# Performance work log

Measured on AMD Instinct MI355X. Metric: run time of the kernel, lower is better.

The kernel has to match this reference:

```python
import jax, jax.numpy as jnp
import numpy as np

EPS = 1e-7  # tf.keras.backend.epsilon()
ROUTINGS = 3


def setup_inputs() -> dict:
    key = jax.random.key(0)
    k1, k2 = jax.random.split(key)
    x = jax.random.normal(k1, (64, 2048, 8), dtype=jnp.float32)
    W = jax.random.normal(k2, (32, 2048, 16, 8), dtype=jnp.float32) * 0.05
    return {"x": x, "W": W}


def _squash(s):
    # source squash: vectors / sqrt(sum(v^2) + eps)
    ssq = jnp.sum(s * s, axis=-1, keepdims=True)
    return s / jnp.sqrt(ssq + EPS)


def reference(x, W):
    # x: [B, N, I]; W: [J, N, D, I]
    # prediction vectors u_hat: [B, J, N, D]
    u_hat = jnp.einsum('bni,jndi->bjnd', x, W)
    b = jnp.zeros(u_hat.shape[:-1], dtype=u_hat.dtype)  # [B, J, N]
    v = None
    for i in range(ROUTINGS):
        c = jax.nn.softmax(b, axis=1)                       # coupling over output caps J
        s = jnp.einsum('bjnd,bjn->bjd', u_hat, c)           # weighted sum over input caps N
        v = _squash(s)                                      # [B, J, D]
        if i < ROUTINGS - 1:
            b = b + jnp.einsum('bjnd,bjd->bjn', u_hat, v)   # agreement update
    return v
```

## Files before the change

kernel.cpp:

```cpp
#include <hip/hip_runtime.h>


#define BB_ 64
#define NN_ 2048
#define II_ 8
#define JJ_ 32
#define DD_ 16
#define NCHUNKS 128
#define CHUNK 16
#define BG 8
#define NBG (BB_ / BG)
#define EPS_ 1e-7f

#define PARTIAL_FLOATS (NCHUNKS * BB_ * JJ_ * DD_)

typedef __attribute__((ext_vector_type(2))) float v2f;

template <int CTRL>
__device__ __forceinline__ float dpp_add(float v) {
  const int s = __builtin_amdgcn_update_dpp(
      0, __builtin_bit_cast(int, v), CTRL, 0xf, 0xf, true);
  return v + __builtin_bit_cast(float, s);
}
#define DPP_QP_XOR1 0xB1
#define DPP_QP_XOR2 0x4E
#define DPP_HALF_MIRROR 0x141
#define DPP_ROR8 0x128

struct W8 {
  v2f k[8];
};

__device__ __forceinline__ W8 loadW(const float* p) {
  const float4* q = (const float4*)p;
  const float4 t0 = q[0], t1 = q[1], t2 = q[2], t3 = q[3];
  W8 w = {{{t0.x, t2.x}, {t0.y, t2.y},
           {t0.z, t2.z}, {t0.w, t2.w},
           {t1.x, t3.x}, {t1.y, t3.y},
           {t1.z, t3.z}, {t1.w, t3.w}}};
  return w;
}

__device__ __forceinline__ void compute_u(const W8& w,
                                          const float (*xs)[CHUNK * II_],
                                          int nl, v2f (&u)[BG]) {
#pragma unroll
  for (int b = 0; b < BG; ++b) {
    const float4* xr = (const float4*)&xs[b][nl * II_];
    const float4 xa = xr[0];
    const float4 xb = xr[1];
    v2f acc = w.k[0] * xa.x;
    acc += w.k[1] * xa.y;
    acc += w.k[2] * xa.z;
    acc += w.k[3] * xa.w;
    acc += w.k[4] * xb.x;
    acc += w.k[5] * xb.y;
    acc += w.k[6] * xb.z;
    acc += w.k[7] * xb.w;
    u[b] = acc;
  }
}

template <int PHASE>
__global__ __launch_bounds__(256, 4) void caps_phase(
    const float* __restrict__ x, const float* __restrict__ W,
    const float* __restrict__ V, float* __restrict__ partial) {
  const int tid = threadIdx.x;
  const int j = tid >> 3;
  const int p = tid & 7;
  const int chunk = blockIdx.x & (NCHUNKS - 1);
  const int bg = blockIdx.x >> 7;
  const int b0 = bg * BG;
  const int n0 = chunk * CHUNK;

  __shared__ float lmat[BG][JJ_];
  __shared__ float cmat[BG][JJ_];
  __shared__ float xs[BG][CHUNK * II_];

  {
    const int b = tid >> 5;
    const int f = (tid & 31) * 4;
    const float4 t =
        *(const float4*)&x[((size_t)(b0 + b) * NN_ + n0) * II_ + f];
    *(float4*)&xs[b][f] = t;
  }

  const float* wp = W + (size_t)j * (NN_ * DD_ * II_) +
                    (size_t)n0 * (DD_ * II_) + (size_t)p * 16;

  float v0r[BG], v1r[BG];
  if (PHASE > 0) {
#pragma unroll
    for (int b = 0; b < BG; ++b) {
      const float2 vv =
          *(const float2*)&V[((size_t)(b0 + b) * JJ_ + j) * DD_ + 2 * p];
      v0r[b] = vv.x;
      v1r[b] = vv.y;
    }
  }

  v2f s[BG];
#pragma unroll
  for (int b = 0; b < BG; ++b) s[b] = (v2f)(0.f);

  W8 wc = loadW(wp);
  __syncthreads();

  for (int nl = 0; nl < CHUNK; ++nl) {
    const int nf = (nl + 1 < CHUNK) ? nl + 1 : nl;
    const W8 wn = loadW(wp + (size_t)nf * 128);

    v2f u[BG];
    compute_u(wc, xs, nl, u);

    if (PHASE == 0) {
#pragma unroll
      for (int b = 0; b < BG; ++b) s[b] += u[b];
    } else {
#pragma unroll
      for (int b = 0; b < BG; ++b) {
        float lp = u[b].x * v0r[b] + u[b].y * v1r[b];
        lp = dpp_add<DPP_QP_XOR1>(lp);
        lp = dpp_add<DPP_QP_XOR2>(lp);
        lp = dpp_add<DPP_HALF_MIRROR>(lp);
        if (p == 0) lmat[b][j] = lp;
      }
      __syncthreads();
      {
        const int jj = tid & 31;
        const int bb = tid >> 5;
        float e0 = __expf(lmat[bb][jj]);
        float m0 = e0;
        m0 = dpp_add<DPP_QP_XOR1>(m0);
        m0 = dpp_add<DPP_QP_XOR2>(m0);
        m0 = dpp_add<DPP_HALF_MIRROR>(m0);
        m0 = dpp_add<DPP_ROR8>(m0);
        m0 += __shfl_xor(m0, 16);
        cmat[bb][jj] = e0 * __builtin_amdgcn_rcpf(m0);
      }
      __syncthreads();
#pragma unroll
      for (int b = 0; b < BG; ++b) {
        const float c = cmat[b][j];
        s[b] += u[b] * c;
      }
    }
    wc = wn;
  }

  const float scale = (PHASE == 0) ? (1.0f / 32.0f) : 1.0f;
#pragma unroll
  for (int b = 0; b < BG; ++b) {
    const size_t off =
        ((size_t)chunk * BB_ + (b0 + b)) * (JJ_ * DD_) + j * DD_ + 2 * p;
    *(float2*)&partial[off] = make_float2(s[b].x * scale, s[b].y * scale);
  }
}

template <int MODE>
__global__ __launch_bounds__(256) void caps_reduce(
    const float* __restrict__ partial, float* __restrict__ V,
    float* __restrict__ out) {
  const int t = blockIdx.x * 256 + threadIdx.x;
  float s = 0.f;
#pragma unroll 16
  for (int c = 0; c < NCHUNKS; ++c)
    s += partial[(size_t)c * (BB_ * JJ_ * DD_) + t];
  float ss = s * s;
  ss += __shfl_xor(ss, 1);
  ss += __shfl_xor(ss, 2);
  ss += __shfl_xor(ss, 4);
  ss += __shfl_xor(ss, 8);
  const float v = s / sqrtf(ss + EPS_);
  if (MODE == 0)
    V[t] = v;
  else if (MODE == 1)
    V[t] += v;
  else
    out[t] = v;
}

extern "C" void kernel_launch(void* const* d_in, const int* in_sizes, int n_in,
                              void* d_out, int out_size, void* d_ws,
                              size_t ws_size, hipStream_t stream) {
  const float* x = (const float*)d_in[0];
  const float* W = (const float*)d_in[1];
  float* out = (float*)d_out;
  float* partial = (float*)d_ws;
  float* V = partial + PARTIAL_FLOATS;

  const dim3 kgrid(NBG * NCHUNKS);
  const dim3 rgrid((BB_ * JJ_ * DD_) / 256);

  caps_phase<0><<<kgrid, 256, 0, stream>>>(x, W, nullptr, partial);
  caps_reduce<0><<<rgrid, 256, 0, stream>>>(partial, V, out);
  caps_phase<1><<<kgrid, 256, 0, stream>>>(x, W, V, partial);
  caps_reduce<1><<<rgrid, 256, 0, stream>>>(partial, V, out);
  caps_phase<2><<<kgrid, 256, 0, stream>>>(x, W, V, partial);
  caps_reduce<2><<<rgrid, 256, 0, stream>>>(partial, V, out);
}
```

Baseline: 187.7 us.

## Halve batch group, double N chunk, and double-buffer W loads two steps ahead

Changes the tiling so each block handles 4 batches over 32 input capsules instead of 8 batches over 16, which halves the partial-sum buffer the reduce kernel reads. The inner loop is unrolled by two so W rows are prefetched two iterations ahead, which hides more global-load latency. The trade-off is that each W element loaded is reused across only 4 batches instead of 8, doubling W traffic from global memory/L2. In phases 1 and 2, only half the threads do the softmax step while the per-step barriers stay in place.

After: 200.4 us. +6.7%, slower.

```diff
diff --git a/kernel.cpp b/kernel.cpp
--- a/kernel.cpp
+++ b/kernel.cpp
@@ -6,9 +6,9 @@
 #define II_ 8
 #define JJ_ 32
 #define DD_ 16
-#define NCHUNKS 128
-#define CHUNK 16
-#define BG 8
+#define NCHUNKS 64
+#define CHUNK 32
+#define BG 4
 #define NBG (BB_ / BG)
 #define EPS_ 1e-7f
 
@@ -69,7 +69,7 @@
   const int j = tid >> 3;
   const int p = tid & 7;
   const int chunk = blockIdx.x & (NCHUNKS - 1);
-  const int bg = blockIdx.x >> 7;
+  const int bg = blockIdx.x / NCHUNKS;
   const int b0 = bg * BG;
   const int n0 = chunk * CHUNK;
 
@@ -78,8 +78,8 @@
   __shared__ float xs[BG][CHUNK * II_];
 
   {
-    const int b = tid >> 5;
-    const int f = (tid & 31) * 4;
+    const int b = tid >> 6;
+    const int f = (tid & 63) * 4;
     const float4 t =
         *(const float4*)&x[((size_t)(b0 + b) * NN_ + n0) * II_ + f];
     *(float4*)&xs[b][f] = t;
@@ -103,49 +103,87 @@
 #pragma unroll
   for (int b = 0; b < BG; ++b) s[b] = (v2f)(0.f);
 
-  W8 wc = loadW(wp);
+  W8 w0 = loadW(wp);
+  W8 w1 = loadW(wp + 128);
   __syncthreads();
 
-  for (int nl = 0; nl < CHUNK; ++nl) {
-    const int nf = (nl + 1 < CHUNK) ? nl + 1 : nl;
-    const W8 wn = loadW(wp + (size_t)nf * 128);
-
-    v2f u[BG];
-    compute_u(wc, xs, nl, u);
-
-    if (PHASE == 0) {
-#pragma unroll
-      for (int b = 0; b < BG; ++b) s[b] += u[b];
-    } else {
-#pragma unroll
-      for (int b = 0; b < BG; ++b) {
-        float lp = u[b].x * v0r[b] + u[b].y * v1r[b];
-        lp = dpp_add<DPP_QP_XOR1>(lp);
-        lp = dpp_add<DPP_QP_XOR2>(lp);
-        lp = dpp_add<DPP_HALF_MIRROR>(lp);
-        if (p == 0) lmat[b][j] = lp;
-      }
-      __syncthreads();
-      {
-        const int jj = tid & 31;
-        const int bb = tid >> 5;
-        float e0 = __expf(lmat[bb][jj]);
-        float m0 = e0;
-        m0 = dpp_add<DPP_QP_XOR1>(m0);
-        m0 = dpp_add<DPP_QP_XOR2>(m0);
-        m0 = dpp_add<DPP_HALF_MIRROR>(m0);
-        m0 = dpp_add<DPP_ROR8>(m0);
-        m0 += __shfl_xor(m0, 16);
-        cmat[bb][jj] = e0 * __builtin_amdgcn_rcpf(m0);
-      }
-      __syncthreads();
-#pragma unroll
-      for (int b = 0; b < BG; ++b) {
-        const float c = cmat[b][j];
-        s[b] += u[b] * c;
+  for (int nl = 0; nl < CHUNK; nl += 2) {
+    const int nf2 = (nl + 2 < CHUNK) ? nl + 2 : CHUNK - 1;
+    const int nf3 = (nl + 3 < CHUNK) ? nl + 3 : CHUNK - 1;
+    const W8 t0 = loadW(wp + (size_t)nf2 * 128);
+
+    {
+      v2f u[BG];
+      compute_u(w0, xs, nl, u);
+      if (PHASE == 0) {
+#pragma unroll
+        for (int b = 0; b < BG; ++b) s[b] += u[b];
+      } else {
+#pragma unroll
+        for (int b = 0; b < BG; ++b) {
+          float lp = u[b].x * v0r[b] + u[b].y * v1r[b];
+          lp = dpp_add<DPP_QP_XOR1>(lp);
+          lp = dpp_add<DPP_QP_XOR2>(lp);
+          lp = dpp_add<DPP_HALF_MIRROR>(lp);
+          if (p == 0) lmat[b][j] = lp;
+        }
+        __syncthreads();
+        if (tid < BG * JJ_) {
+          const int jj = tid & 31;
+          const int bb = tid >> 5;
+          float e0 = __expf(lmat[bb][jj]);
+          float m0 = e0;
+          m0 = dpp_add<DPP_QP_XOR1>(m0);
+          m0 = dpp_add<DPP_QP_XOR2>(m0);
+          m0 = dpp_add<DPP_HALF_MIRROR>(m0);
+          m0 = dpp_add<DPP_ROR8>(m0);
+          m0 += __shfl_xor(m0, 16);
+          cmat[bb][jj] = e0 * __builtin_amdgcn_rcpf(m0);
+        }
+        __syncthreads();
+#pragma unroll
+        for (int b = 0; b < BG; ++b) s[b] += u[b] * cmat[b][j];
       }
     }
-    wc = wn;
+
+    const W8 t1 = loadW(wp + (size_t)nf3 * 128);
+
+    {
+      v2f u[BG];
+      compute_u(w1, xs, nl + 1, u);
+      if (PHASE == 0) {
+#pragma unroll
+        for (int b = 0; b < BG; ++b) s[b] += u[b];
+      } else {
+#pragma unroll
+        for (int b = 0; b < BG; ++b) {
+          float lp = u[b].x * v0r[b] + u[b].y * v1r[b];
+          lp = dpp_add<DPP_QP_XOR1>(lp);
+          lp = dpp_add<DPP_QP_XOR2>(lp);
+          lp = dpp_add<DPP_HALF_MIRROR>(lp);
+          if (p == 0) lmat[b][j] = lp;
+        }
+        __syncthreads();
+        if (tid < BG * JJ_) {
+          const int jj = tid & 31;
+          const int bb = tid >> 5;
+          float e0 = __expf(lmat[bb][jj]);
+          float m0 = e0;
+          m0 = dpp_add<DPP_QP_XOR1>(m0);
+          m0 = dpp_add<DPP_QP_XOR2>(m0);
+          m0 = dpp_add<DPP_HALF_MIRROR>(m0);
+          m0 = dpp_add<DPP_ROR8>(m0);
+          m0 += __shfl_xor(m0, 16);
+          cmat[bb][jj] = e0 * __builtin_amdgcn_rcpf(m0);
+        }
+        __syncthreads();
+#pragma unroll
+        for (int b = 0; b < BG; ++b) s[b] += u[b] * cmat[b][j];
+      }
+    }
+
+    w0 = t0;
+    w1 = t1;
   }
 
   const float scale = (PHASE == 0) ? (1.0f / 32.0f) : 1.0f;
```
